# Performance work log

Hardware: AMD Instinct MI355X
Metric: run time of the kernel (lower is better)

## Reference

```python
import jax, jax.numpy as jnp
import numpy as np

TAU = 0.1
N, D, NUM_CLASSES = 4096, 512, 100


def setup_inputs() -> dict:
    key = jax.random.key(0)
    k1, k2 = jax.random.split(key)
    features = jax.random.normal(k1, (N, D), dtype=jnp.float32)
    targets = jax.random.randint(k2, (N,), 0, NUM_CLASSES, dtype=jnp.int64)
    return {"features": features, "targets": targets}


def reference(features, targets):
    n = features.shape[0]
    # pairwise cosine similarity (with torch-style zero-norm guard)
    sim_mat = features @ features.T                      # [N, N]
    norms = jnp.linalg.norm(features, axis=1)            # [N]
    norm_mat = norms[:, None] * norms[None, :]           # [N, N]
    norm_mat = jnp.where(norm_mat == 0, 1e-8, norm_mat)
    norm_sim = sim_mat / norm_mat
    # positive-pair mask: same class (includes diagonal)
    mask = (targets[None, :] == targets[:, None]).astype(norm_sim.dtype)  # [N, N]
    exp_mat = jnp.exp(norm_sim / TAU)
    eye = jnp.eye(n, dtype=exp_mat.dtype)
    # triu(.,1) + tril(.,-1) == zero out the diagonal
    actual_sim = exp_mat * (1.0 - eye)
    # per-row sum over negatives (mask == 0)
    neg_sum = (actual_sim * (1.0 - mask)).sum(axis=1, keepdims=True)      # [N, 1]
    normalised = actual_sim / (actual_sim + neg_sum) + eye
    positive_cardinality = mask.sum(axis=1, keepdims=True)                # [N, 1]
    loss_mat = -jnp.log(normalised) / positive_cardinality
    loss_mat = jnp.where(jnp.isnan(loss_mat), 0.0, loss_mat)
    contrastive_loss = (loss_mat * mask).sum() / positive_cardinality.sum()
    return contrastive_loss
```

## Files before the change

kernel.cpp:

```cpp
#include <hip/hip_runtime.h>
#include <hip/hip_bf16.h>
#include <math.h>

#define NROWS 4096
#define DIM   512
#define MAXP  128
#define TAU_INV 10.0f

using short8 = __attribute__((ext_vector_type(8))) short;
using f32x4  = __attribute__((ext_vector_type(4))) float;

#define OFF_FNB   0
#define OFF_NEG   4194304
#define OFF_RANK  (OFF_NEG + 16384)
#define OFF_SMALL (OFF_RANK + 16384)
#define OFF_HIST  (OFF_SMALL)
#define OFF_DONE  (OFF_SMALL + 512)
#define OFF_PN    (OFF_SMALL + 768)
#define OFF_PD    (OFF_SMALL + 1024)
#define OFF_PV    (OFF_SMALL + 2048)

#define GLOBAL_AS __attribute__((address_space(1)))
#define LDS_AS    __attribute__((address_space(3)))

__device__ __forceinline__ void gload_lds16(const void* g, void* l) {
    __builtin_amdgcn_global_load_lds((const GLOBAL_AS unsigned int*)g,
                                     (LDS_AS unsigned int*)l, 16, 0, 0);
}

__device__ __forceinline__ unsigned short f32_to_bf16_rn(float x) {
    unsigned int u = __float_as_uint(x);
    unsigned int r = u + 0x7FFFu + ((u >> 16) & 1u);
    return (unsigned short)(r >> 16);
}

__global__ void k_norm(const float* __restrict__ feat, const int* __restrict__ tgt,
                       unsigned short* __restrict__ fnb, int* __restrict__ hist,
                       int* __restrict__ rank, int* __restrict__ zero_base) {
    int tid = threadIdx.x;
    if (blockIdx.x < 16) zero_base[blockIdx.x * 256 + tid] = 0;
    int wid = tid >> 6, l = tid & 63;
    int row = blockIdx.x * 4 + wid;
    if (l == 0) rank[row] = atomicAdd(&hist[tgt[row]], 1);
    const float4* src = (const float4*)(feat + (size_t)row * DIM);
    float4 v0 = src[l * 2];
    float4 v1 = src[l * 2 + 1];
    float ss = v0.x*v0.x + v0.y*v0.y + v0.z*v0.z + v0.w*v0.w
             + v1.x*v1.x + v1.y*v1.y + v1.z*v1.z + v1.w*v1.w;
    #pragma unroll
    for (int m = 1; m < 64; m <<= 1) ss += __shfl_xor(ss, m);
    float rs = rsqrtf(fmaxf(ss, 1e-30f));
    float f[8] = { v0.x*rs, v0.y*rs, v0.z*rs, v0.w*rs,
                   v1.x*rs, v1.y*rs, v1.z*rs, v1.w*rs };
    uint4 o;
    o.x = (unsigned)f32_to_bf16_rn(f[0]) | ((unsigned)f32_to_bf16_rn(f[1]) << 16);
    o.y = (unsigned)f32_to_bf16_rn(f[2]) | ((unsigned)f32_to_bf16_rn(f[3]) << 16);
    o.z = (unsigned)f32_to_bf16_rn(f[4]) | ((unsigned)f32_to_bf16_rn(f[5]) << 16);
    o.w = (unsigned)f32_to_bf16_rn(f[6]) | ((unsigned)f32_to_bf16_rn(f[7]) << 16);
    ((uint4*)fnb)[row * 64 + l] = o;
}

__global__ __launch_bounds__(256, 4)
void k_main(const unsigned short* __restrict__ fnb, const int* __restrict__ tgt,
            const int* __restrict__ rank,
            float* __restrict__ negsum, float* __restrict__ posvals)
{
    __shared__ uint4 As4[1024];
    __shared__ uint4 Bs4[1024];
    __shared__ int clsI[128], clsJ[128];
    __shared__ int rkI[128],  rkJ[128];

    int b = blockIdx.x;
    int bi = 0, rem = b;
    while (rem >= 32 - bi) { rem -= 32 - bi; bi++; }
    int bj = bi + rem;
    bool diag = (bi == bj);
    int i0 = bi * 128, j0 = bj * 128;

    int tid = threadIdx.x;
    if (tid < 128) { clsI[tid] = tgt[i0 + tid];        rkI[tid] = rank[i0 + tid]; }
    else           { clsJ[tid-128] = tgt[j0 + tid-128]; rkJ[tid-128] = rank[j0 + tid-128]; }

    int wid = tid >> 6, l = tid & 63;
    int wr = wid >> 1, wc = wid & 1;

    f32x4 acc[4][4];
    #pragma unroll
    for (int a = 0; a < 4; a++)
        #pragma unroll
        for (int bq = 0; bq < 4; bq++)
            acc[a][bq] = (f32x4){0.f, 0.f, 0.f, 0.f};

    const uint4* gA = (const uint4*)fnb;
    const uint4* Bbase = diag ? As4 : Bs4;

    for (int kt = 0; kt < 8; kt++) {
        #pragma unroll
        for (int p = 0; p < 4; p++) {
            int id = p * 256 + tid;
            int row = id >> 3, cx = id & 7;
            int c = cx ^ (row & 7);
            gload_lds16(&gA[(i0 + row) * 64 + kt * 8 + c], &As4[id]);
            if (!diag)
                gload_lds16(&gA[(j0 + row) * 64 + kt * 8 + c], &Bs4[id]);
        }
        __syncthreads();
        #pragma unroll
        for (int s = 0; s < 2; s++) {
            short8 af[4], bf[4];
            #pragma unroll
            for (int mi = 0; mi < 4; mi++) {
                int row = wr * 64 + mi * 16 + (l & 15);
                int cx = (s * 4 + (l >> 4)) ^ (row & 7);
                af[mi] = *(const short8*)&As4[row * 8 + cx];
            }
            #pragma unroll
            for (int ni = 0; ni < 4; ni++) {
                int row = wc * 64 + ni * 16 + (l & 15);
                int cx = (s * 4 + (l >> 4)) ^ (row & 7);
                bf[ni] = *(const short8*)&Bbase[row * 8 + cx];
            }
            #pragma unroll
            for (int mi = 0; mi < 4; mi++)
                #pragma unroll
                for (int ni = 0; ni < 4; ni++)
                    acc[mi][ni] = __builtin_amdgcn_mfma_f32_16x16x32_bf16(
                        af[mi], bf[ni], acc[mi][ni], 0, 0, 0);
        }
        __syncthreads();
    }

    int cj[4], gj[4], rj[4];
    #pragma unroll
    for (int ni = 0; ni < 4; ni++) {
        int jl = wc * 64 + ni * 16 + (l & 15);
        cj[ni] = clsJ[jl];
        gj[ni] = j0 + jl;
        rj[ni] = rkJ[jl];
    }
    float ns[4][4];
    float cns[4] = {0.f, 0.f, 0.f, 0.f};
    #pragma unroll
    for (int mi = 0; mi < 4; mi++) {
        #pragma unroll
        for (int r = 0; r < 4; r++) {
            int il = wr * 64 + mi * 16 + ((l >> 4) << 2) + r;
            int ci = clsI[il];
            int ri = rkI[il];
            int gi = i0 + il;
            float nacc = 0.f;
            #pragma unroll
            for (int ni = 0; ni < 4; ni++) {
                float p = acc[mi][ni][r] * TAU_INV;
                float e = __expf(p);
                if (ci != cj[ni]) {
                    nacc += e;
                    cns[ni] += e;
                } else if (gi != gj[ni]) {
                    posvals[(size_t)gi * MAXP + rj[ni]] = p;
                    if (!diag)
                        posvals[(size_t)gj[ni] * MAXP + ri] = p;
                }
            }
            ns[mi][r] = nacc;
        }
    }
    #pragma unroll
    for (int mi = 0; mi < 4; mi++) {
        #pragma unroll
        for (int r = 0; r < 4; r++) {
            float v = ns[mi][r];
            v += __shfl_xor(v, 1);
            v += __shfl_xor(v, 2);
            v += __shfl_xor(v, 4);
            v += __shfl_xor(v, 8);
            if ((l & 15) == 0) {
                int il = wr * 64 + mi * 16 + ((l >> 4) << 2) + r;
                atomicAdd(&negsum[i0 + il], v);
            }
        }
    }
    if (!diag) {
        #pragma unroll
        for (int ni = 0; ni < 4; ni++) {
            float v = cns[ni];
            v += __shfl_xor(v, 16);
            v += __shfl_xor(v, 32);
            if (l < 16) atomicAdd(&negsum[gj[ni]], v);
        }
    }
}

__global__ void k_fin(const float* __restrict__ negsum, const int* __restrict__ tgt,
                      const int* __restrict__ rank, const int* __restrict__ hist,
                      const float* __restrict__ posvals,
                      float* __restrict__ partialN, float* __restrict__ partialD,
                      int* __restrict__ done, float* __restrict__ out)
{
    __shared__ float redN[4], redD[4];
    __shared__ int lastflag;
    int tid = threadIdx.x, w = tid >> 6, l = tid & 63;
    int base = (blockIdx.x * 4 + w) * 16;
    float Sv[16]; int cv[16], rv[16];
    #pragma unroll
    for (int it = 0; it < 16; it++) {
        int row = base + it;
        Sv[it] = negsum[row];
        cv[it] = hist[tgt[row]];
        rv[it] = rank[row];
    }
    float nacc = 0.f, dacc = 0.f;
    #pragma unroll
    for (int it = 0; it < 16; it++) {
        int row = base + it;
        const float* pv = posvals + (size_t)row * MAXP;
        float p0 = pv[l];
        float p1 = pv[l + 64];
        float S = Sv[it]; int card = cv[it], rk = rv[it];
        float t0 = __logf(__expf(p0) + S) - p0;
        float t1 = __logf(__expf(p1) + S) - p1;
        float t = ((l < card && l != rk) ? t0 : 0.f)
                + ((l + 64 < card && l + 64 != rk) ? t1 : 0.f);
        nacc += t / (float)card;
        if (l == 0) dacc += (float)card;
    }
    #pragma unroll
    for (int msk = 1; msk < 64; msk <<= 1) {
        nacc += __shfl_xor(nacc, msk);
        dacc += __shfl_xor(dacc, msk);
    }
    if (l == 0) { redN[w] = nacc; redD[w] = dacc; }
    __syncthreads();
    if (tid == 0) {
        partialN[blockIdx.x] = redN[0] + redN[1] + redN[2] + redN[3];
        partialD[blockIdx.x] = redD[0] + redD[1] + redD[2] + redD[3];
        __threadfence();
        int d = atomicAdd(done, 1);
        lastflag = (d == (int)gridDim.x - 1) ? 1 : 0;
    }
    __syncthreads();
    if (lastflag && tid < 64) {
        __threadfence();
        float n = partialN[tid];
        float dd = partialD[tid];
        #pragma unroll
        for (int msk = 1; msk < 64; msk <<= 1) {
            n  += __shfl_xor(n, msk);
            dd += __shfl_xor(dd, msk);
        }
        if (tid == 0) out[0] = n / dd;
    }
}

extern "C" void kernel_launch(void* const* d_in, const int* in_sizes, int n_in,
                              void* d_out, int out_size, void* d_ws, size_t ws_size,
                              hipStream_t stream) {
    (void)in_sizes; (void)n_in; (void)out_size; (void)ws_size;
    const float* feat = (const float*)d_in[0];
    const int*   tgt  = (const int*)d_in[1];
    float* out = (float*)d_out;
    char* ws = (char*)d_ws;

    unsigned short* fnb = (unsigned short*)(ws + OFF_FNB);
    float* negsum  = (float*)(ws + OFF_NEG);
    int*   rank    = (int*)(ws + OFF_RANK);
    int*   hist    = (int*)(ws + OFF_HIST);
    int*   done    = (int*)(ws + OFF_DONE);
    float* pN      = (float*)(ws + OFF_PN);
    float* pD      = (float*)(ws + OFF_PD);
    float* posvals = (float*)(ws + OFF_PV);

    hipMemsetAsync(ws + OFF_SMALL, 0, 768, stream);

    k_norm<<<dim3(1024), dim3(256), 0, stream>>>(feat, tgt, fnb, hist, rank,
                                                 (int*)(ws + OFF_NEG));
    k_main<<<dim3(528), dim3(256), 0, stream>>>(fnb, tgt, rank, negsum, posvals);
    k_fin<<<dim3(64), dim3(256), 0, stream>>>(negsum, tgt, rank, hist, posvals,
                                              pN, pD, done, out);
}
```

Baseline: 102.5 us.

## Fuse finalize into main kernel via completion counter; compute class counts by scan

Removes the memset and the separate finalize launch. The last 64 blocks to finish the GEMM tile work spin-wait on a global counter and then do the per-row log reduction, with a second counter for the final sum. Rank and cardinality are now computed deterministically by each row scanning all targets instead of atomic histogramming, which also drops the memset dependency. This trades launch overhead for spin-waiting blocks and redundant target scans; it relies on the waiting blocks not starving the unfinished ones.

```diff
diff --git a/kernel.cpp b/kernel.cpp
--- a/kernel.cpp
+++ b/kernel.cpp
@@ -6,19 +6,21 @@
 #define DIM   512
 #define MAXP  128
 #define TAU_INV 10.0f
+#define TOT   528
+#define FINB  64
+#define FIN_START (TOT - FINB)
 
 using short8 = __attribute__((ext_vector_type(8))) short;
 using f32x4  = __attribute__((ext_vector_type(4))) float;
 
 #define OFF_FNB   0
 #define OFF_NEG   4194304
-#define OFF_RANK  (OFF_NEG + 16384)
-#define OFF_SMALL (OFF_RANK + 16384)
-#define OFF_HIST  (OFF_SMALL)
-#define OFF_DONE  (OFF_SMALL + 512)
-#define OFF_PN    (OFF_SMALL + 768)
-#define OFF_PD    (OFF_SMALL + 1024)
-#define OFF_PV    (OFF_SMALL + 2048)
+#define OFF_RANK  (OFF_NEG  + 16384)
+#define OFF_CARD  (OFF_RANK + 16384)
+#define OFF_DONE  (OFF_CARD + 16384)
+#define OFF_PN    (OFF_DONE + 256)
+#define OFF_PD    (OFF_PN   + 256)
+#define OFF_PV    (OFF_PD   + 256)
 
 #define GLOBAL_AS __attribute__((address_space(1)))
 #define LDS_AS    __attribute__((address_space(3)))
@@ -34,14 +36,29 @@
     return (unsigned short)(r >> 16);
 }
 
-__global__ void k_norm(const float* __restrict__ feat, const int* __restrict__ tgt,
-                       unsigned short* __restrict__ fnb, int* __restrict__ hist,
-                       int* __restrict__ rank, int* __restrict__ zero_base) {
+__global__ void k_prep(const float* __restrict__ feat, const int* __restrict__ tgt,
+                       unsigned short* __restrict__ fnb,
+                       int* __restrict__ rank, int* __restrict__ card,
+                       float* __restrict__ negsum, int* __restrict__ done) {
     int tid = threadIdx.x;
-    if (blockIdx.x < 16) zero_base[blockIdx.x * 256 + tid] = 0;
-    int wid = tid >> 6, l = tid & 63;
-    int row = blockIdx.x * 4 + wid;
-    if (l == 0) rank[row] = atomicAdd(&hist[tgt[row]], 1);
+    if (blockIdx.x < 4) ((float4*)negsum)[blockIdx.x * 256 + tid] = make_float4(0.f,0.f,0.f,0.f);
+    if (blockIdx.x == 4 && tid < 2) done[tid] = 0;
+    int w = tid >> 6, l = tid & 63;
+    int row = blockIdx.x * 4 + w;
+    int myc = tgt[row];
+    int call = 0, clt = 0;
+    for (int it = 0; it < 64; it++) {
+        int j = it * 64 + l;
+        int t = tgt[j];
+        call += (t == myc);
+        clt  += (t == myc && j < row) ? 1 : 0;
+    }
+    #pragma unroll
+    for (int m = 1; m < 64; m <<= 1) {
+        call += __shfl_xor(call, m);
+        clt  += __shfl_xor(clt, m);
+    }
+    if (l == 0) { card[row] = call; rank[row] = clt; }
     const float4* src = (const float4*)(feat + (size_t)row * DIM);
     float4 v0 = src[l * 2];
     float4 v1 = src[l * 2 + 1];
@@ -61,14 +78,22 @@
 }
 
 __global__ __launch_bounds__(256, 4)
-void k_main(const unsigned short* __restrict__ fnb, const int* __restrict__ tgt,
-            const int* __restrict__ rank,
-            float* __restrict__ negsum, float* __restrict__ posvals)
+void k_mainfin(const unsigned short* __restrict__ fnb, const int* __restrict__ tgt,
+               const int* __restrict__ rank, const int* __restrict__ card,
+               float* __restrict__ negsum, float* __restrict__ posvals,
+               int* __restrict__ done,
+               float* __restrict__ partialN, float* __restrict__ partialD,
+               float* __restrict__ out)
 {
     __shared__ uint4 As4[1024];
     __shared__ uint4 Bs4[1024];
     __shared__ int clsI[128], clsJ[128];
     __shared__ int rkI[128],  rkJ[128];
+    __shared__ int sd;
+    __shared__ float redN[4], redD[4];
+    __shared__ int lastflag;
+
+    int tid = threadIdx.x, w = tid >> 6, l = tid & 63;
 
     int b = blockIdx.x;
     int bi = 0, rem = b;
@@ -77,12 +102,10 @@
     bool diag = (bi == bj);
     int i0 = bi * 128, j0 = bj * 128;
 
-    int tid = threadIdx.x;
-    if (tid < 128) { clsI[tid] = tgt[i0 + tid];        rkI[tid] = rank[i0 + tid]; }
-    else           { clsJ[tid-128] = tgt[j0 + tid-128]; rkJ[tid-128] = rank[j0 + tid-128]; }
-
-    int wid = tid >> 6, l = tid & 63;
-    int wr = wid >> 1, wc = wid & 1;
+    if (tid < 128) { clsI[tid] = tgt[i0 + tid];             rkI[tid] = rank[i0 + tid]; }
+    else           { clsJ[tid-128] = tgt[j0 + tid-128];     rkJ[tid-128] = rank[j0 + tid-128]; }
+
+    int wr = w >> 1, wc = w & 1;
 
     f32x4 acc[4][4];
     #pragma unroll
@@ -189,66 +212,72 @@
             if (l < 16) atomicAdd(&negsum[gj[ni]], v);
         }
     }
-}
-
-__global__ void k_fin(const float* __restrict__ negsum, const int* __restrict__ tgt,
-                      const int* __restrict__ rank, const int* __restrict__ hist,
-                      const float* __restrict__ posvals,
-                      float* __restrict__ partialN, float* __restrict__ partialD,
-                      int* __restrict__ done, float* __restrict__ out)
-{
-    __shared__ float redN[4], redD[4];
-    __shared__ int lastflag;
-    int tid = threadIdx.x, w = tid >> 6, l = tid & 63;
-    int base = (blockIdx.x * 4 + w) * 16;
-    float Sv[16]; int cv[16], rv[16];
-    #pragma unroll
-    for (int it = 0; it < 16; it++) {
-        int row = base + it;
-        Sv[it] = negsum[row];
-        cv[it] = hist[tgt[row]];
-        rv[it] = rank[row];
-    }
-    float nacc = 0.f, dacc = 0.f;
-    #pragma unroll
-    for (int it = 0; it < 16; it++) {
-        int row = base + it;
-        const float* pv = posvals + (size_t)row * MAXP;
-        float p0 = pv[l];
-        float p1 = pv[l + 64];
-        float S = Sv[it]; int card = cv[it], rk = rv[it];
-        float t0 = __logf(__expf(p0) + S) - p0;
-        float t1 = __logf(__expf(p1) + S) - p1;
-        float t = ((l < card && l != rk) ? t0 : 0.f)
-                + ((l + 64 < card && l + 64 != rk) ? t1 : 0.f);
-        nacc += t / (float)card;
-        if (l == 0) dacc += (float)card;
-    }
-    #pragma unroll
-    for (int msk = 1; msk < 64; msk <<= 1) {
-        nacc += __shfl_xor(nacc, msk);
-        dacc += __shfl_xor(dacc, msk);
-    }
-    if (l == 0) { redN[w] = nacc; redD[w] = dacc; }
+
+    __threadfence();
     __syncthreads();
+    if (tid == 0) sd = atomicAdd(&done[0], 1);
+    __syncthreads();
+    int d = sd;
+    if (d < FIN_START) return;
+
+    int chunk = d - FIN_START;
     if (tid == 0) {
-        partialN[blockIdx.x] = redN[0] + redN[1] + redN[2] + redN[3];
-        partialD[blockIdx.x] = redD[0] + redD[1] + redD[2] + redD[3];
-        __threadfence();
-        int d = atomicAdd(done, 1);
-        lastflag = (d == (int)gridDim.x - 1) ? 1 : 0;
+        while (atomicAdd(&done[0], 0) < TOT) __builtin_amdgcn_s_sleep(16);
     }
     __syncthreads();
-    if (lastflag && tid < 64) {
-        __threadfence();
-        float n = partialN[tid];
-        float dd = partialD[tid];
+    __threadfence();
+
+    {
+        int base = (chunk * 4 + w) * 16;
+        float Sv[16]; int cv[16], rv[16];
+        #pragma unroll
+        for (int it = 0; it < 16; it++) {
+            int row = base + it;
+            Sv[it] = negsum[row];
+            cv[it] = card[row];
+            rv[it] = rank[row];
+        }
+        float nacc = 0.f, dacc = 0.f;
+        #pragma unroll
+        for (int it = 0; it < 16; it++) {
+            int row = base + it;
+            const float* pv = posvals + (size_t)row * MAXP;
+            float p0 = pv[l];
+            float p1 = pv[l + 64];
+            float S = Sv[it]; int cd = cv[it], rk = rv[it];
+            float t0 = __logf(__expf(p0) + S) - p0;
+            float t1 = __logf(__expf(p1) + S) - p1;
+            float t = ((l < cd && l != rk) ? t0 : 0.f)
+                    + ((l + 64 < cd && l + 64 != rk) ? t1 : 0.f);
+            nacc += t / (float)cd;
+            if (l == 0) dacc += (float)cd;
+        }
         #pragma unroll
         for (int msk = 1; msk < 64; msk <<= 1) {
-            n  += __shfl_xor(n, msk);
-            dd += __shfl_xor(dd, msk);
-        }
-        if (tid == 0) out[0] = n / dd;
+            nacc += __shfl_xor(nacc, msk);
+            dacc += __shfl_xor(dacc, msk);
+        }
+        if (l == 0) { redN[w] = nacc; redD[w] = dacc; }
+        __syncthreads();
+        if (tid == 0) {
+            partialN[chunk] = redN[0] + redN[1] + redN[2] + redN[3];
+            partialD[chunk] = redD[0] + redD[1] + redD[2] + redD[3];
+            __threadfence();
+            int d2 = atomicAdd(&done[1], 1);
+            lastflag = (d2 == FINB - 1) ? 1 : 0;
+        }
+        __syncthreads();
+        if (lastflag && tid < 64) {
+            __threadfence();
+            float n = partialN[tid];
+            float dd = partialD[tid];
+            #pragma unroll
+            for (int msk = 1; msk < 64; msk <<= 1) {
+                n  += __shfl_xor(n, msk);
+                dd += __shfl_xor(dd, msk);
+            }
+            if (tid == 0) out[0] = n / dd;
+        }
     }
 }
 
@@ -264,17 +293,15 @@
     unsigned short* fnb = (unsigned short*)(ws + OFF_FNB);
     float* negsum  = (float*)(ws + OFF_NEG);
     int*   rank    = (int*)(ws + OFF_RANK);
-    int*   hist    = (int*)(ws + OFF_HIST);
+    int*   card    = (int*)(ws + OFF_CARD);
     int*   done    = (int*)(ws + OFF_DONE);
     float* pN      = (float*)(ws + OFF_PN);
     float* pD      = (float*)(ws + OFF_PD);
     float* posvals = (float*)(ws + OFF_PV);
 
-    hipMemsetAsync(ws + OFF_SMALL, 0, 768, stream);
-
-    k_norm<<<dim3(1024), dim3(256), 0, stream>>>(feat, tgt, fnb, hist, rank,
-                                                 (int*)(ws + OFF_NEG));
-    k_main<<<dim3(528), dim3(256), 0, stream>>>(fnb, tgt, rank, negsum, posvals);
-    k_fin<<<dim3(64), dim3(256), 0, stream>>>(negsum, tgt, rank, hist, posvals,
-                                              pN, pD, done, out);
-}
+    k_prep<<<dim3(1024), dim3(256), 0, stream>>>(feat, tgt, fnb, rank, card,
+                                                 negsum, done);
+    k_mainfin<<<dim3(TOT), dim3(256), 0, stream>>>(fnb, tgt, rank, card,
+                                                   negsum, posvals, done,
+                                                   pN, pD, out);
+}
```

New measurement: 135.8 us. 32.4% more time.

## Load MFMA operands directly from global memory and remap tile order

Applied to the files above, without the earlier changes.

The GEMM main loop no longer stages A/B tiles in LDS through global_load_lds with barriers. Each wave now reads its bf16 fragments straight from global memory into registers, relying on L1/L2 caches for reuse. The block index is also permuted so that consecutive blocks map to spread-out triangular tiles (an XCD-aware remap). Launch bounds drop to 2 blocks per CU to allow more registers. The trade is that the barriers go away, but each wave now issues redundant global loads that were previously shared through LDS.

```diff
diff --git a/kernel.cpp b/kernel.cpp
--- a/kernel.cpp
+++ b/kernel.cpp
@@ -6,27 +6,22 @@
 #define DIM   512
 #define MAXP  128
 #define TAU_INV 10.0f
+#define NPAN  32
+#define TOT   (NPAN*(NPAN+1)/2)
+#define CPX   (TOT/8)
 
 using short8 = __attribute__((ext_vector_type(8))) short;
 using f32x4  = __attribute__((ext_vector_type(4))) float;
 
 #define OFF_FNB   0
 #define OFF_NEG   4194304
-#define OFF_RANK  (OFF_NEG + 16384)
+#define OFF_RANK  (OFF_NEG  + 16384)
 #define OFF_SMALL (OFF_RANK + 16384)
 #define OFF_HIST  (OFF_SMALL)
 #define OFF_DONE  (OFF_SMALL + 512)
 #define OFF_PN    (OFF_SMALL + 768)
 #define OFF_PD    (OFF_SMALL + 1024)
 #define OFF_PV    (OFF_SMALL + 2048)
-
-#define GLOBAL_AS __attribute__((address_space(1)))
-#define LDS_AS    __attribute__((address_space(3)))
-
-__device__ __forceinline__ void gload_lds16(const void* g, void* l) {
-    __builtin_amdgcn_global_load_lds((const GLOBAL_AS unsigned int*)g,
-                                     (LDS_AS unsigned int*)l, 16, 0, 0);
-}
 
 __device__ __forceinline__ unsigned short f32_to_bf16_rn(float x) {
     unsigned int u = __float_as_uint(x);
@@ -60,26 +55,27 @@
     ((uint4*)fnb)[row * 64 + l] = o;
 }
 
-__global__ __launch_bounds__(256, 4)
+__global__ __launch_bounds__(256, 2)
 void k_main(const unsigned short* __restrict__ fnb, const int* __restrict__ tgt,
             const int* __restrict__ rank,
             float* __restrict__ negsum, float* __restrict__ posvals)
 {
-    __shared__ uint4 As4[1024];
-    __shared__ uint4 Bs4[1024];
     __shared__ int clsI[128], clsJ[128];
     __shared__ int rkI[128],  rkJ[128];
 
-    int b = blockIdx.x;
+    int bid = blockIdx.x;
+    int b = (bid & 7) * CPX + (bid >> 3);
+
     int bi = 0, rem = b;
-    while (rem >= 32 - bi) { rem -= 32 - bi; bi++; }
+    while (rem >= NPAN - bi) { rem -= NPAN - bi; bi++; }
     int bj = bi + rem;
     bool diag = (bi == bj);
     int i0 = bi * 128, j0 = bj * 128;
 
     int tid = threadIdx.x;
-    if (tid < 128) { clsI[tid] = tgt[i0 + tid];        rkI[tid] = rank[i0 + tid]; }
-    else           { clsJ[tid-128] = tgt[j0 + tid-128]; rkJ[tid-128] = rank[j0 + tid-128]; }
+    if (tid < 128) { clsI[tid] = tgt[i0 + tid];             rkI[tid] = rank[i0 + tid]; }
+    else           { clsJ[tid-128] = tgt[j0 + tid-128];     rkJ[tid-128] = rank[j0 + tid-128]; }
+    __syncthreads();
 
     int wid = tid >> 6, l = tid & 63;
     int wr = wid >> 1, wc = wid & 1;
@@ -92,34 +88,28 @@
             acc[a][bq] = (f32x4){0.f, 0.f, 0.f, 0.f};
 
     const uint4* gA = (const uint4*)fnb;
-    const uint4* Bbase = diag ? As4 : Bs4;
-
+    int c0 = (l >> 4);
+
+    int arow[4], brow[4];
+    #pragma unroll
+    for (int mi = 0; mi < 4; mi++)
+        arow[mi] = (i0 + wr * 64 + mi * 16 + (l & 15)) * 64;
+    #pragma unroll
+    for (int ni = 0; ni < 4; ni++)
+        brow[ni] = (j0 + wc * 64 + ni * 16 + (l & 15)) * 64;
+
+    #pragma unroll 2
     for (int kt = 0; kt < 8; kt++) {
         #pragma unroll
-        for (int p = 0; p < 4; p++) {
-            int id = p * 256 + tid;
-            int row = id >> 3, cx = id & 7;
-            int c = cx ^ (row & 7);
-            gload_lds16(&gA[(i0 + row) * 64 + kt * 8 + c], &As4[id]);
-            if (!diag)
-                gload_lds16(&gA[(j0 + row) * 64 + kt * 8 + c], &Bs4[id]);
-        }
-        __syncthreads();
-        #pragma unroll
         for (int s = 0; s < 2; s++) {
+            int c = kt * 8 + s * 4 + c0;
             short8 af[4], bf[4];
             #pragma unroll
-            for (int mi = 0; mi < 4; mi++) {
-                int row = wr * 64 + mi * 16 + (l & 15);
-                int cx = (s * 4 + (l >> 4)) ^ (row & 7);
-                af[mi] = *(const short8*)&As4[row * 8 + cx];
-            }
-            #pragma unroll
-            for (int ni = 0; ni < 4; ni++) {
-                int row = wc * 64 + ni * 16 + (l & 15);
-                int cx = (s * 4 + (l >> 4)) ^ (row & 7);
-                bf[ni] = *(const short8*)&Bbase[row * 8 + cx];
-            }
+            for (int mi = 0; mi < 4; mi++)
+                af[mi] = *(const short8*)&gA[arow[mi] + c];
+            #pragma unroll
+            for (int ni = 0; ni < 4; ni++)
+                bf[ni] = *(const short8*)&gA[brow[ni] + c];
             #pragma unroll
             for (int mi = 0; mi < 4; mi++)
                 #pragma unroll
@@ -127,7 +117,6 @@
                     acc[mi][ni] = __builtin_amdgcn_mfma_f32_16x16x32_bf16(
                         af[mi], bf[ni], acc[mi][ni], 0, 0, 0);
         }
-        __syncthreads();
     }
 
     int cj[4], gj[4], rj[4];
@@ -216,13 +205,13 @@
         const float* pv = posvals + (size_t)row * MAXP;
         float p0 = pv[l];
         float p1 = pv[l + 64];
-        float S = Sv[it]; int card = cv[it], rk = rv[it];
+        float S = Sv[it]; int cd = cv[it], rk = rv[it];
         float t0 = __logf(__expf(p0) + S) - p0;
         float t1 = __logf(__expf(p1) + S) - p1;
-        float t = ((l < card && l != rk) ? t0 : 0.f)
-                + ((l + 64 < card && l + 64 != rk) ? t1 : 0.f);
-        nacc += t / (float)card;
-        if (l == 0) dacc += (float)card;
+        float t = ((l < cd && l != rk) ? t0 : 0.f)
+                + ((l + 64 < cd && l + 64 != rk) ? t1 : 0.f);
+        nacc += t / (float)cd;
+        if (l == 0) dacc += (float)cd;
     }
     #pragma unroll
     for (int msk = 1; msk < 64; msk <<= 1) {
@@ -274,7 +263,7 @@
 
     k_norm<<<dim3(1024), dim3(256), 0, stream>>>(feat, tgt, fnb, hist, rank,
                                                  (int*)(ws + OFF_NEG));
-    k_main<<<dim3(528), dim3(256), 0, stream>>>(fnb, tgt, rank, negsum, posvals);
+    k_main<<<dim3(TOT), dim3(256), 0, stream>>>(fnb, tgt, rank, negsum, posvals);
     k_fin<<<dim3(64), dim3(256), 0, stream>>>(negsum, tgt, rank, hist, posvals,
                                               pN, pD, done, out);
 }
```

Result: slower. 136.0 us (+32.7%).
